# Kernel tuning notes

Measured on AMD Instinct MI355X. Metric: run time of the kernel, lower is better.

The kernel has to match this reference:

```python
import jax, jax.numpy as jnp
import numpy as np
from jax import lax

NUM_CHANNELS = 3
NUM_HEADS = 8
PATCH = 16  # projection_dim = 3 * 16 * 16 = 768
EPS = 1e-5


def setup_inputs() -> dict:
    key = jax.random.key(0)
    ks = jax.random.split(key, 16)
    B, N, D, Hdim = 4, 1024, 768, 3072
    H = NUM_HEADS

    def init(k, shape, fan_in):
        bound = 1.0 / np.sqrt(fan_in)
        return jax.random.uniform(k, shape, jnp.float32, -bound, bound)

    return {
        "x": jax.random.normal(ks[0], (B, N, D), jnp.float32),
        # 3x3 conv QKV projections over per-patch [3,16,16] images (no bias, qkv_bias=False)
        "qconv_w": init(ks[1], (NUM_CHANNELS, NUM_CHANNELS, 3, 3), NUM_CHANNELS * 9),
        "kconv_w": init(ks[2], (NUM_CHANNELS, NUM_CHANNELS, 3, 3), NUM_CHANNELS * 9),
        "vconv_w": init(ks[3], (NUM_CHANNELS, NUM_CHANNELS, 3, 3), NUM_CHANNELS * 9),
        # 1x1 conv mixing heads of the attention map + BatchNorm2d(heads)
        "reatten_w": init(ks[4], (H, H), H),
        "reatten_b": init(ks[5], (H,), H),
        "bn_g": jnp.ones((H,), jnp.float32),
        "bn_b": jnp.zeros((H,), jnp.float32),
        # output projection (Linear dim->dim)
        "proj_w": init(ks[6], (D, D), D),
        "proj_b": init(ks[7], (D,), D),
        # LayerNorm over (num_patches, projection_dim) jointly
        "ln_g": jnp.ones((N, D), jnp.float32),
        "ln_b": jnp.zeros((N, D), jnp.float32),
        # FeedForward
        "ff_w1": init(ks[8], (Hdim, D), D),
        "ff_b1": init(ks[9], (Hdim,), D),
        "ff_w2": init(ks[10], (D, Hdim), Hdim),
        "ff_b2": init(ks[11], (D,), Hdim),
    }


def _conv3x3(x, w):
    # x: [BN, C, p, p], w: [C, C, 3, 3], stride 1, SAME padding
    return lax.conv_general_dilated(x, w, (1, 1), "SAME",
                                    dimension_numbers=("NCHW", "OIHW", "NCHW"))


def _layernorm_2d(x, g, b):
    # LayerNorm over last two axes (N, D) jointly, biased variance, eps=1e-5
    mu = jnp.mean(x, axis=(-2, -1), keepdims=True)
    var = jnp.mean(jnp.square(x - mu), axis=(-2, -1), keepdims=True)
    return (x - mu) * lax.rsqrt(var + EPS) * g + b


def _encoder_fwd(x, qconv_w, kconv_w, vconv_w, reatten_w, reatten_b,
                 bn_g, bn_b, proj_w, proj_b, ln_g, ln_b,
                 ff_w1, ff_b1, ff_w2, ff_b2):
    B, N, D = x.shape
    H = NUM_HEADS
    hd = D // H
    scale = hd ** -0.5

    # --- ReAttention ---
    xi = x.reshape(B * N, NUM_CHANNELS, PATCH, PATCH)

    def qkv(w):
        y = _conv3x3(xi, w).reshape(B, N, H, hd)
        return y.transpose(0, 2, 1, 3)  # [B, H, N, hd]

    q, k, v = qkv(qconv_w), qkv(kconv_w), qkv(vconv_w)

    attn = jax.nn.softmax(jnp.einsum("bhnd,bhmd->bhnm", q, k) * scale, axis=-1)

    # learned cross-head 1x1 conv + BatchNorm2d (training-mode batch stats)
    attn = jnp.einsum("gh,bhnm->bgnm", reatten_w, attn) + reatten_b[None, :, None, None]
    mu = jnp.mean(attn, axis=(0, 2, 3), keepdims=True)
    var = jnp.mean(jnp.square(attn - mu), axis=(0, 2, 3), keepdims=True)
    attn = (attn - mu) * lax.rsqrt(var + EPS)
    attn = attn * bn_g[None, :, None, None] + bn_b[None, :, None, None]

    out = jnp.einsum("bhnm,bhmd->bhnd", attn, v)
    out = out.transpose(0, 2, 1, 3).reshape(B, N, D)
    out = out @ proj_w.T + proj_b

    # --- residual + LN ---
    x1 = _layernorm_2d(x + out, ln_g, ln_b)

    # --- FeedForward (exact GELU) + residual + LN ---
    h = jax.nn.gelu(x1 @ ff_w1.T + ff_b1, approximate=False)
    ff = h @ ff_w2.T + ff_b2
    return _layernorm_2d(x1 + ff, ln_g, ln_b)


def reference(x, qconv_w, kconv_w, vconv_w, reatten_w, reatten_b,
              bn_g, bn_b, proj_w, proj_b, ln_g, ln_b,
              ff_w1, ff_b1, ff_w2, ff_b2):
    return _encoder_fwd(x, qconv_w, kconv_w, vconv_w, reatten_w, reatten_b,
                        bn_g, bn_b, proj_w, proj_b, ln_g, ln_b,
                        ff_w1, ff_b1, ff_w2, ff_b2)
```

## Files before the change

kernel.cpp:

```cpp
#include <hip/hip_runtime.h>
#include <math.h>


typedef unsigned short u16;
typedef unsigned int u32;
typedef __bf16 bf16x8 __attribute__((ext_vector_type(8)));
typedef float f32x4 __attribute__((ext_vector_type(4)));

#define EPSV 1e-5f
#define SL2E 0.14724444620253177f
#define EXPC -11.541560327111707f

__device__ __forceinline__ u16 f2bf(float f) {
  union { float f; u32 u; } v; v.f = f;
  u32 u = v.u + 0x7fffu + ((v.u >> 16) & 1u);
  return (u16)(u >> 16);
}
__device__ __forceinline__ float bf2f(u16 h) {
  union { u32 u; float f; } v; v.u = ((u32)h) << 16; return v.f;
}
__device__ __forceinline__ f32x4 mfma16(bf16x8 a, bf16x8 b, f32x4 c) {
  return __builtin_amdgcn_mfma_f32_16x16x32_bf16(a, b, c, 0, 0, 0);
}
__device__ __forceinline__ void gload16(const void* gp, void* lp) {
  __builtin_amdgcn_global_load_lds(
      (const __attribute__((address_space(1))) u32*)gp,
      (__attribute__((address_space(3))) u32*)lp, 16, 0, 0);
}

__global__ __launch_bounds__(256) void k_f2b(const float* __restrict__ s,
                                             u16* __restrict__ d, int n) {
  int i = blockIdx.x * 256 + threadIdx.x;
  int stride = gridDim.x * 256;
  for (; i < n; i += stride) d[i] = f2bf(s[i]);
}

__global__ __launch_bounds__(256) void k_conv(const float* __restrict__ x,
    const float* __restrict__ wq, const float* __restrict__ wk, const float* __restrict__ wv,
    u16* __restrict__ qhi, u16* __restrict__ qlo,
    u16* __restrict__ khi, u16* __restrict__ klo,
    float* __restrict__ vb)
{
  __shared__ float patch[768], swq[81], swk[81], swv[81];
  int bid = blockIdx.x;
  int b = bid >> 10, n = bid & 1023;
  int t = threadIdx.x;
  const float* xr = x + (size_t)bid * 768;
  patch[t] = xr[t]; patch[t + 256] = xr[t + 256]; patch[t + 512] = xr[t + 512];
  if (t < 81) { swq[t] = wq[t]; swk[t] = wk[t]; swv[t] = wv[t]; }
  __syncthreads();
  #pragma unroll
  for (int r = 0; r < 3; ++r) {
    int f = t + 256 * r;
    int o = f >> 8, rem = f & 255, pp = rem >> 4, qq = rem & 15;
    float aq = 0.f, ak = 0.f, av = 0.f;
    #pragma unroll
    for (int i = 0; i < 3; ++i)
      #pragma unroll
      for (int dp = 0; dp < 3; ++dp) {
        int ip = pp + dp - 1;
        if (ip < 0 || ip > 15) continue;
        #pragma unroll
        for (int dq = 0; dq < 3; ++dq) {
          int iq = qq + dq - 1;
          if (iq < 0 || iq > 15) continue;
          float pv = patch[i * 256 + ip * 16 + iq];
          int wi = ((o * 3 + i) * 3 + dp) * 3 + dq;
          aq += swq[wi] * pv; ak += swk[wi] * pv; av += swv[wi] * pv;
        }
      }
    int h = f / 96, d = f - h * 96;
    size_t oi = ((size_t)(b * 8 + h) * 1024 + n) * 96 + d;
    float aqs = aq * SL2E;
    u16 qh_ = f2bf(aqs); qhi[oi] = qh_; qlo[oi] = f2bf(aqs - bf2f(qh_));
    u16 kh_ = f2bf(ak);  khi[oi] = kh_; klo[oi] = f2bf(ak - bf2f(kh_));
    vb[oi] = av;
  }
}

__global__ __launch_bounds__(256) void k_vtr(const float* __restrict__ vb,
                                             u16* __restrict__ vtr)
{
  __shared__ u16 lds[12288];
  int bid = blockIdx.x;
  int bh = bid >> 3, n0 = (bid & 7) * 128;
  int t = threadIdx.x;
  int n = t >> 1, dh = (t & 1) * 48;
  const float* src = vb + ((size_t)bh * 1024 + n0 + n) * 96 + dh;
  #pragma unroll
  for (int j4 = 0; j4 < 12; ++j4) {
    float4 v = *(const float4*)(src + j4 * 4);
    int d = dh + j4 * 4;
    lds[(d + 0) * 128 + n] = f2bf(v.x);
    lds[(d + 1) * 128 + n] = f2bf(v.y);
    lds[(d + 2) * 128 + n] = f2bf(v.z);
    lds[(d + 3) * 128 + n] = f2bf(v.w);
  }
  __syncthreads();
  #pragma unroll
  for (int j = 0; j < 48; ++j) {
    int flat = t + 256 * j;
    int d = flat >> 7, n2 = flat & 127;
    vtr[((size_t)bh * 96 + d) * 1024 + n0 + n2] = lds[flat];
  }
}

#define LOADK(KH, KL, M)                                            \
  {                                                                 \
    size_t ko_ = (kbase + (M) + l15) * 96 + (size_t)(lhi * 8);      \
    _Pragma("unroll")                                               \
    for (int kk = 0; kk < 3; ++kk) {                                \
      KH[kk] = *(const bf16x8*)(khi + ko_ + kk * 32);               \
      KL[kk] = *(const bf16x8*)(klo + ko_ + kk * 32);               \
    }                                                               \
  }

__global__ __launch_bounds__(256, 4) void k_passA(
    const u16* __restrict__ qhi, const u16* __restrict__ qlo,
    const u16* __restrict__ khi, const u16* __restrict__ klo,
    float* __restrict__ zp)
{
  int bid = blockIdx.x;
  int bh = bid >> 6, rest = bid & 63, tile = rest >> 2, qtr = rest & 3;
  int t = threadIdx.x, lane = t & 63, wv = t >> 6;
  int l15 = lane & 15, lhi = lane >> 4;
  int n0 = tile * 64 + wv * 16;
  size_t qoff = ((size_t)bh * 1024 + n0 + l15) * 96 + lhi * 8;
  bf16x8 qh[3], ql[3];
  #pragma unroll
  for (int kk = 0; kk < 3; ++kk) {
    qh[kk] = *(const bf16x8*)(qhi + qoff + kk * 32);
    ql[kk] = *(const bf16x8*)(qlo + qoff + kk * 32);
  }
  size_t kbase = (size_t)bh * 1024;
  float z[4] = {0.f, 0.f, 0.f, 0.f};
  bf16x8 khA[3], klA[3], khB[3], klB[3];
  int m0 = qtr * 256;
  LOADK(khA, klA, m0)
  for (int it = 0; it < 8; ++it) {
    int mb = m0 + it * 32;
    LOADK(khB, klB, mb + 16)
    {
      f32x4 C = {0.f, 0.f, 0.f, 0.f};
      #pragma unroll
      for (int kk = 0; kk < 3; ++kk) {
        C = mfma16(qh[kk], khA[kk], C);
        C = mfma16(qh[kk], klA[kk], C);
        C = mfma16(ql[kk], khA[kk], C);
      }
      #pragma unroll
      for (int r = 0; r < 4; ++r) z[r] += exp2f(C[r] + EXPC);
    }
    if (it < 7) LOADK(khA, klA, mb + 32)
    {
      f32x4 C = {0.f, 0.f, 0.f, 0.f};
      #pragma unroll
      for (int kk = 0; kk < 3; ++kk) {
        C = mfma16(qh[kk], khB[kk], C);
        C = mfma16(qh[kk], klB[kk], C);
        C = mfma16(ql[kk], khB[kk], C);
      }
      #pragma unroll
      for (int r = 0; r < 4; ++r) z[r] += exp2f(C[r] + EXPC);
    }
  }
  #pragma unroll
  for (int off = 1; off < 16; off <<= 1)
    #pragma unroll
    for (int r = 0; r < 4; ++r) z[r] += __shfl_xor(z[r], off);
  if (l15 == 0) {
    #pragma unroll
    for (int r = 0; r < 4; ++r)
      zp[qtr * 32768 + bh * 1024 + n0 + lhi * 4 + r] = z[r];
  }
}

__global__ __launch_bounds__(256) void k_zmerge(const float* __restrict__ zp,
                                                float* __restrict__ invZ)
{
  int idx = blockIdx.x * 256 + threadIdx.x;
  float z = zp[idx] + zp[32768 + idx] + zp[65536 + idx] + zp[98304 + idx];
  invZ[idx] = 1.f / z;
}

__global__ __launch_bounds__(512, 4) void k_passB(
    const u16* __restrict__ qhi, const u16* __restrict__ qlo,
    const u16* __restrict__ khi, const u16* __restrict__ klo,
    const u16* __restrict__ vtr, const float* __restrict__ invZ,
    const float* __restrict__ rw,
    float* __restrict__ U0, float* __restrict__ U1,
    float* __restrict__ U2, float* __restrict__ U3,
    float* __restrict__ pstat)
{
  __shared__ u16 clds[32768];
  int bid = blockIdx.x;
  int b = bid >> 8, rest = bid & 255, nt = rest >> 2, mq = rest & 3;
  int n0 = nt * 16;
  int t = threadIdx.x, lane = t & 63, w = t >> 6;
  int l15 = lane & 15, lhi = lane >> 4;
  int mbase = mq * 256 + w * 32;
  int mrow0 = mbase + ((l15 >> 2) * 8) + (l15 & 3);

  float cm[8][8];
  #pragma unroll
  for (int g = 0; g < 8; ++g) {
    float wsum = 0.f;
    #pragma unroll
    for (int h = 0; h < 8; ++h) wsum += rw[g * 8 + h];
    float cg = -wsum * (1.f / 1024.f);
    #pragma unroll
    for (int jj = 0; jj < 8; ++jj) cm[g][jj] = cg;
  }

  #pragma unroll 1
  for (int h = 0; h < 8; ++h) {
    size_t base = (size_t)(b * 8 + h) * 1024;
    const u16* qhp = qhi + (base + n0 + l15) * 96 + lhi * 8;
    const u16* qlp = qlo + (base + n0 + l15) * 96 + lhi * 8;
    const u16* khp = khi + (base + mrow0) * 96 + lhi * 8;
    const u16* klp = klo + (base + mrow0) * 96 + lhi * 8;
    f32x4 C0 = {0.f, 0.f, 0.f, 0.f}, C1 = {0.f, 0.f, 0.f, 0.f};
    #pragma unroll
    for (int kk = 0; kk < 3; ++kk) {
      bf16x8 qh8 = *(const bf16x8*)(qhp + kk * 32);
      bf16x8 ql8 = *(const bf16x8*)(qlp + kk * 32);
      bf16x8 kh0 = *(const bf16x8*)(khp + kk * 32);
      bf16x8 kl0 = *(const bf16x8*)(klp + kk * 32);
      bf16x8 kh1 = *(const bf16x8*)(khp + 384 + kk * 32);
      bf16x8 kl1 = *(const bf16x8*)(klp + 384 + kk * 32);
      C0 = mfma16(kh0, qh8, C0);
      C0 = mfma16(kl0, qh8, C0);
      C0 = mfma16(kh0, ql8, C0);
      C1 = mfma16(kh1, qh8, C1);
      C1 = mfma16(kl1, qh8, C1);
      C1 = mfma16(kh1, ql8, C1);
    }
    float iz = invZ[base + n0 + l15];
    #pragma unroll
    for (int r = 0; r < 4; ++r) {
      float p0 = exp2f(C0[r] + EXPC) * iz;
      float p1 = exp2f(C1[r] + EXPC) * iz;
      #pragma unroll
      for (int g = 0; g < 8; ++g) {
        float wgh = rw[g * 8 + h];
        cm[g][r]     += wgh * p0;
        cm[g][4 + r] += wgh * p1;
      }
    }
  }

  {
    float sc[8], scc[8];
    #pragma unroll
    for (int g = 0; g < 8; ++g) {
      float s = 0.f, ss = 0.f;
      #pragma unroll
      for (int jj = 0; jj < 8; ++jj) { float v = cm[g][jj]; s += v; ss += v * v; }
      sc[g] = s; scc[g] = ss;
    }
    #pragma unroll
    for (int off = 32; off > 0; off >>= 1)
      #pragma unroll
      for (int g = 0; g < 8; ++g) {
        sc[g] += __shfl_down(sc[g], off);
        scc[g] += __shfl_down(scc[g], off);
      }
    if (lane == 0) {
      #pragma unroll
      for (int g = 0; g < 8; ++g) {
        pstat[(size_t)(bid * 8 + w) * 16 + g] = sc[g];
        pstat[(size_t)(bid * 8 + w) * 16 + 8 + g] = scc[g];
      }
    }
  }

  #pragma unroll
  for (int g = 0; g < 8; ++g) {
    union { u16 us[8]; bf16x8 bv; } pk;
    #pragma unroll
    for (int jj = 0; jj < 8; ++jj) pk.us[jj] = f2bf(cm[g][jj]);
    *(bf16x8*)&clds[((w * 8 + g) * 64 + lane) * 8] = pk.bv;
  }
  __syncthreads();

  f32x4 acc[6];
  #pragma unroll
  for (int ds = 0; ds < 6; ++ds) acc[ds] = (f32x4){0.f, 0.f, 0.f, 0.f};
  size_t vbase = (size_t)(b * 8 + w) * 96;
  for (int mc = 0; mc < 8; ++mc) {
    bf16x8 af = *(const bf16x8*)&clds[((mc * 8 + w) * 64 + lane) * 8];
    int mof = mq * 256 + mc * 32 + lhi * 8;
    #pragma unroll
    for (int ds = 0; ds < 6; ++ds) {
      bf16x8 vf = *(const bf16x8*)(vtr + (vbase + ds * 16 + l15) * 1024 + mof);
      acc[ds] = mfma16(af, vf, acc[ds]);
    }
  }
  float* Uq = (mq == 0) ? U0 : (mq == 1) ? U1 : (mq == 2) ? U2 : U3;
  #pragma unroll
  for (int ds = 0; ds < 6; ++ds)
    #pragma unroll
    for (int r = 0; r < 4; ++r) {
      int n = lhi * 4 + r;
      Uq[((size_t)(b * 1024 + n0 + n)) * 768 + w * 96 + ds * 16 + l15] = acc[ds][r];
    }
}

__global__ __launch_bounds__(384) void k_vcs(const float* __restrict__ vb,
                                             float* __restrict__ vcs)
{
  __shared__ float part[4][96];
  int bh = blockIdx.x, t = threadIdx.x;
  int c = t % 96, g4 = t / 96;
  float a = 0.f;
  const float* vp = vb + (size_t)bh * 98304 + (size_t)g4 * 24576 + c;
  for (int m = 0; m < 256; ++m) a += vp[m * 96];
  part[g4][c] = a;
  __syncthreads();
  if (t < 96) vcs[bh * 96 + t] = part[0][t] + part[1][t] + part[2][t] + part[3][t];
}

__global__ __launch_bounds__(256) void k_statred1(const float* __restrict__ pstat,
                                                  float* __restrict__ pred)
{
  __shared__ float part[16][17];
  int bb = blockIdx.x, t = threadIdx.x;
  int j = t >> 4, s = t & 15;
  float a = 0.f;
  #pragma unroll
  for (int k2 = 0; k2 < 8; ++k2)
    a += pstat[(size_t)(bb * 128 + s + 16 * k2) * 16 + j];
  part[j][s] = a;
  __syncthreads();
  if (t < 16) {
    float v = 0.f;
    #pragma unroll
    for (int s2 = 0; s2 < 16; ++s2) v += part[t][s2];
    pred[bb * 16 + t] = v;
  }
}

__global__ __launch_bounds__(256) void k_statred2(const float* __restrict__ pred,
                                                  float* __restrict__ stats)
{
  __shared__ float part[16][17];
  int t = threadIdx.x;
  int j = t >> 4, s = t & 15;
  float a = 0.f;
  #pragma unroll
  for (int k2 = 0; k2 < 4; ++k2)
    a += pred[(size_t)(s + 16 * k2) * 16 + j];
  part[j][s] = a;
  __syncthreads();
  if (t < 16) {
    float v = 0.f;
    #pragma unroll
    for (int s2 = 0; s2 < 16; ++s2) v += part[t][s2];
    stats[t] = v;
  }
}

__global__ __launch_bounds__(256) void k_bnfin(const float* __restrict__ U0,
    const float* __restrict__ U1, const float* __restrict__ U2,
    const float* __restrict__ U3, const float* __restrict__ vcs,
    const float* __restrict__ stats, const float* __restrict__ bng,
    const float* __restrict__ bnb, u16* __restrict__ ubb)
{
  size_t idx = (size_t)blockIdx.x * 256 + threadIdx.x;
  int col = (int)(idx % 768); int i = (int)(idx / 768); int b = i >> 10;
  int g = col / 96, d = col - g * 96;
  const float cnt = 4194304.f;
  float mc = stats[g] / cnt;
  float var = stats[8 + g] / cnt - mc * mc;
  float sg = bng[g] * rsqrtf(var + EPSV);
  float tg = bnb[g] - sg * mc;
  float u = (U0[idx] + U1[idx]) + (U2[idx] + U3[idx]);
  ubb[idx] = f2bf(sg * u + tg * vcs[(b * 8 + g) * 96 + d]);
}

template<int GELU_, int RES_, int STATS_, int BF16OUT>
__global__ __launch_bounds__(256) void k_gemm(
    const u16* __restrict__ A, const u16* __restrict__ W,
    const float* __restrict__ bias, const float* __restrict__ res,
    float* __restrict__ out, u16* __restrict__ outb,
    int K, int Nc, float* __restrict__ stats)
{
  __shared__ u16 As[8192], Bs[8192];
  __shared__ float red[8];
  int t = threadIdx.x, lane = t & 63, wv = t >> 6;
  int l15 = lane & 15, lhi = lane >> 4;
  int i0 = blockIdx.y * 128, j0 = blockIdx.x * 128;
  int wr = wv >> 1, wc = wv & 1;
  f32x4 acc[4][4];
  #pragma unroll
  for (int mi = 0; mi < 4; ++mi)
    #pragma unroll
    for (int ni = 0; ni < 4; ++ni) acc[mi][ni] = (f32x4){0.f, 0.f, 0.f, 0.f};
  int rA = lane >> 3;
  int colel = 8 * ((lane & 7) ^ rA);
  for (int k0 = 0; k0 < K; k0 += 64) {
    if (k0) __syncthreads();
    #pragma unroll
    for (int i = 0; i < 4; ++i) {
      int cA = wv * 4 + i;
      int r = cA * 8 + rA;
      gload16(A + (size_t)(i0 + r) * K + k0 + colel, &As[cA * 512]);
      gload16(W + (size_t)(j0 + r) * K + k0 + colel, &Bs[cA * 512]);
    }
    __syncthreads();
    #pragma unroll
    for (int ks = 0; ks < 2; ++ks) {
      bf16x8 af[4], bf[4];
      #pragma unroll
      for (int mi = 0; mi < 4; ++mi) {
        int r2 = wr * 64 + mi * 16 + l15;
        af[mi] = *(const bf16x8*)&As[r2 * 64 + ((ks * 32 + lhi * 8) ^ (8 * (r2 & 7)))];
      }
      #pragma unroll
      for (int ni = 0; ni < 4; ++ni) {
        int r3 = wc * 64 + ni * 16 + l15;
        bf[ni] = *(const bf16x8*)&Bs[r3 * 64 + ((ks * 32 + lhi * 8) ^ (8 * (r3 & 7)))];
      }
      #pragma unroll
      for (int mi = 0; mi < 4; ++mi)
        #pragma unroll
        for (int ni = 0; ni < 4; ++ni)
          acc[mi][ni] = mfma16(af[mi], bf[ni], acc[mi][ni]);
    }
  }
  float ls = 0.f, lss = 0.f;
  #pragma unroll
  for (int mi = 0; mi < 4; ++mi) {
    #pragma unroll
    for (int ni = 0; ni < 4; ++ni) {
      int col = j0 + wc * 64 + ni * 16 + l15;
      float bv = bias[col];
      #pragma unroll
      for (int r = 0; r < 4; ++r) {
        int row = i0 + wr * 64 + mi * 16 + lhi * 4 + r;
        float val = acc[mi][ni][r] + bv;
        if (RES_) val += res[(size_t)row * Nc + col];
        if (GELU_) val = 0.5f * val * (1.f + erff(val * 0.70710678118654752f));
        if (BF16OUT) outb[(size_t)row * Nc + col] = f2bf(val);
        else out[(size_t)row * Nc + col] = val;
        if (STATS_) { ls += val; lss += val * val; }
      }
    }
  }
  if (STATS_) {
    #pragma unroll
    for (int off = 32; off > 0; off >>= 1) {
      ls += __shfl_down(ls, off); lss += __shfl_down(lss, off);
    }
    if (lane == 0) { red[wv * 2] = ls; red[wv * 2 + 1] = lss; }
    __syncthreads();
    if (t == 0) {
      int b = i0 >> 10;
      atomicAdd(&stats[b * 2],     red[0] + red[2] + red[4] + red[6]);
      atomicAdd(&stats[b * 2 + 1], red[1] + red[3] + red[5] + red[7]);
    }
  }
}

template<int BF16OUT>
__global__ __launch_bounds__(256) void k_ln(const float* __restrict__ y,
    const float* __restrict__ stats, const float* __restrict__ g,
    const float* __restrict__ bta, float* __restrict__ outp, u16* __restrict__ outb)
{
  size_t idx = (size_t)blockIdx.x * 256 + threadIdx.x;
  int i = (int)(idx / 768), col = (int)(idx % 768);
  int b = i >> 10, n = i & 1023;
  const float cnt = 786432.f;
  float mu = stats[b * 2] / cnt;
  float var = stats[b * 2 + 1] / cnt - mu * mu;
  float r = rsqrtf(var + EPSV);
  size_t gi = (size_t)n * 768 + col;
  float v = (y[idx] - mu) * r * g[gi] + bta[gi];
  outp[idx] = v;
  if (BF16OUT) outb[idx] = f2bf(v);
}

extern "C" void kernel_launch(void* const* d_in, const int* in_sizes, int n_in,
                              void* d_out, int out_size, void* d_ws, size_t ws_size,
                              hipStream_t stream)
{
  const float* x   = (const float*)d_in[0];
  const float* qw  = (const float*)d_in[1];
  const float* kw  = (const float*)d_in[2];
  const float* vw  = (const float*)d_in[3];
  const float* rw  = (const float*)d_in[4];
  const float* bng = (const float*)d_in[6];
  const float* bnb = (const float*)d_in[7];
  const float* pw  = (const float*)d_in[8];
  const float* pb  = (const float*)d_in[9];
  const float* lng = (const float*)d_in[10];
  const float* lnb = (const float*)d_in[11];
  const float* fw1 = (const float*)d_in[12];
  const float* fb1 = (const float*)d_in[13];
  const float* fw2 = (const float*)d_in[14];
  const float* fb2 = (const float*)d_in[15];
  float* out = (float*)d_out;

  float* ws    = (float*)d_ws;
  float* stats = ws;
  float* pstat = ws + 64;
  float* vcs   = ws + 131136;
  float* zp    = ws + 134208;
  float* invZ  = ws + 265280;
  float* vb    = ws + 298048;
  float* U0    = ws + 3443776;
  float* U1    = ws + 6589504;
  float* x1    = ws + 9735232;
  u16* u16b = (u16*)(ws + 12880960);
  u16* qhi  = u16b;
  u16* qlo  = u16b + 3145728;
  u16* khi  = u16b + 6291456;
  u16* klo  = u16b + 9437184;
  u16* vtr  = u16b + 12582912;
  u16* ubb  = u16b + 15728640;
  u16* pwb  = u16b + 18874368;
  u16* fw1b = u16b + 19464192;
  u16* fw2b = u16b + 21823488;
  float* U2 = vb;
  float* U3 = x1;
  float* pred = zp;
  u16* x1b = qhi;
  u16* hb  = qlo;
  float* y1 = U0;
  float* y2 = vb;

  hipMemsetAsync(stats, 0, 64 * sizeof(float), stream);
  k_f2b<<<1024, 256, 0, stream>>>(pw, pwb, 589824);
  k_f2b<<<2048, 256, 0, stream>>>(fw1, fw1b, 2359296);
  k_f2b<<<2048, 256, 0, stream>>>(fw2, fw2b, 2359296);

  k_conv<<<4096, 256, 0, stream>>>(x, qw, kw, vw, qhi, qlo, khi, klo, vb);
  k_passA<<<2048, 256, 0, stream>>>(qhi, qlo, khi, klo, zp);
  k_vtr<<<256, 256, 0, stream>>>(vb, vtr);
  k_vcs<<<32, 384, 0, stream>>>(vb, vcs);
  k_zmerge<<<128, 256, 0, stream>>>(zp, invZ);
  k_passB<<<1024, 512, 0, stream>>>(qhi, qlo, khi, klo, vtr, invZ, rw,
                                    U0, U1, U2, U3, pstat);
  k_statred1<<<64, 256, 0, stream>>>(pstat, pred);
  k_statred2<<<1, 256, 0, stream>>>(pred, stats);
  k_bnfin<<<12288, 256, 0, stream>>>(U0, U1, U2, U3, vcs, stats, bng, bnb, ubb);

  k_gemm<0,1,1,0><<<dim3(6, 32), 256, 0, stream>>>(ubb, pwb, pb, x, y1, nullptr, 768, 768, stats + 16);
  k_ln<1><<<12288, 256, 0, stream>>>(y1, stats + 16, lng, lnb, x1, x1b);
  k_gemm<1,0,0,1><<<dim3(24, 32), 256, 0, stream>>>(x1b, fw1b, fb1, nullptr, nullptr, hb, 768, 3072, nullptr);
  k_gemm<0,1,1,0><<<dim3(6, 32), 256, 0, stream>>>(hb, fw2b, fb2, x1, y2, nullptr, 3072, 768, stats + 24);
  k_ln<0><<<12288, 256, 0, stream>>>(y2, stats + 24, lng, lnb, out, nullptr);
}
```

Baseline: 373.4 us.

## Stage per-head probabilities in LDS and apply head mixing per output head

The passB kernel no longer keeps an 8x8 per-thread accumulator for all mixed heads across the head loop. Each wave now writes bf16 softmax probabilities for every head into LDS. Each wave then computes its own mixed head by combining the 8 heads per m-chunk just before the PV MFMA, which cuts register pressure and the 8x FMA fan-out per probability. The BatchNorm partial statistics become one value per wave per block, so the first stat-reduction kernel is simplified. The cost is that probabilities are rounded to bf16 before mixing rather than after, which adds a rounding step, and more LDS reads happen in the inner loop.

```diff
diff --git a/kernel.cpp b/kernel.cpp
--- a/kernel.cpp
+++ b/kernel.cpp
@@ -192,7 +192,7 @@
     float* __restrict__ U2, float* __restrict__ U3,
     float* __restrict__ pstat)
 {
-  __shared__ u16 clds[32768];
+  __shared__ u16 plds[32768];
   int bid = blockIdx.x;
   int b = bid >> 8, rest = bid & 255, nt = rest >> 2, mq = rest & 3;
   int n0 = nt * 16;
@@ -200,17 +200,6 @@
   int l15 = lane & 15, lhi = lane >> 4;
   int mbase = mq * 256 + w * 32;
   int mrow0 = mbase + ((l15 >> 2) * 8) + (l15 & 3);
-
-  float cm[8][8];
-  #pragma unroll
-  for (int g = 0; g < 8; ++g) {
-    float wsum = 0.f;
-    #pragma unroll
-    for (int h = 0; h < 8; ++h) wsum += rw[g * 8 + h];
-    float cg = -wsum * (1.f / 1024.f);
-    #pragma unroll
-    for (int jj = 0; jj < 8; ++jj) cm[g][jj] = cg;
-  }
 
   #pragma unroll 1
   for (int h = 0; h < 8; ++h) {
@@ -236,66 +225,64 @@
       C1 = mfma16(kh1, ql8, C1);
     }
     float iz = invZ[base + n0 + l15];
+    union { u16 us[8]; bf16x8 bv; } pk;
     #pragma unroll
     for (int r = 0; r < 4; ++r) {
-      float p0 = exp2f(C0[r] + EXPC) * iz;
-      float p1 = exp2f(C1[r] + EXPC) * iz;
-      #pragma unroll
-      for (int g = 0; g < 8; ++g) {
-        float wgh = rw[g * 8 + h];
-        cm[g][r]     += wgh * p0;
-        cm[g][4 + r] += wgh * p1;
-      }
-    }
-  }
-
-  {
-    float sc[8], scc[8];
-    #pragma unroll
-    for (int g = 0; g < 8; ++g) {
-      float s = 0.f, ss = 0.f;
-      #pragma unroll
-      for (int jj = 0; jj < 8; ++jj) { float v = cm[g][jj]; s += v; ss += v * v; }
-      sc[g] = s; scc[g] = ss;
-    }
-    #pragma unroll
-    for (int off = 32; off > 0; off >>= 1)
-      #pragma unroll
-      for (int g = 0; g < 8; ++g) {
-        sc[g] += __shfl_down(sc[g], off);
-        scc[g] += __shfl_down(scc[g], off);
-      }
-    if (lane == 0) {
-      #pragma unroll
-      for (int g = 0; g < 8; ++g) {
-        pstat[(size_t)(bid * 8 + w) * 16 + g] = sc[g];
-        pstat[(size_t)(bid * 8 + w) * 16 + 8 + g] = scc[g];
-      }
-    }
-  }
-
-  #pragma unroll
-  for (int g = 0; g < 8; ++g) {
+      pk.us[r]     = f2bf(exp2f(C0[r] + EXPC) * iz);
+      pk.us[4 + r] = f2bf(exp2f(C1[r] + EXPC) * iz);
+    }
+    *(bf16x8*)&plds[((w * 8 + h) * 64 + lane) * 8] = pk.bv;
+  }
+  __syncthreads();
+
+  float wg[8];
+  #pragma unroll
+  for (int h = 0; h < 8; ++h) wg[h] = rw[w * 8 + h];
+  float cg = -(((wg[0] + wg[1]) + (wg[2] + wg[3])) +
+               ((wg[4] + wg[5]) + (wg[6] + wg[7]))) * (1.f / 1024.f);
+  f32x4 acc[6];
+  #pragma unroll
+  for (int ds = 0; ds < 6; ++ds) acc[ds] = (f32x4){0.f, 0.f, 0.f, 0.f};
+  float sc = 0.f, scc = 0.f;
+  size_t vbase = (size_t)(b * 8 + w) * 96;
+  #pragma unroll 1
+  for (int mc = 0; mc < 8; ++mc) {
+    float cm8[8];
+    #pragma unroll
+    for (int jj = 0; jj < 8; ++jj) cm8[jj] = cg;
+    #pragma unroll
+    for (int h = 0; h < 8; ++h) {
+      union { u32 ud[4]; bf16x8 bv; } pf;
+      pf.bv = *(const bf16x8*)&plds[((mc * 8 + h) * 64 + lane) * 8];
+      float wgh = wg[h];
+      #pragma unroll
+      for (int k2 = 0; k2 < 4; ++k2) {
+        union { u32 u; float f; } lo, hi;
+        lo.u = pf.ud[k2] << 16;
+        hi.u = pf.ud[k2] & 0xffff0000u;
+        cm8[2 * k2]     += wgh * lo.f;
+        cm8[2 * k2 + 1] += wgh * hi.f;
+      }
+    }
     union { u16 us[8]; bf16x8 bv; } pk;
     #pragma unroll
-    for (int jj = 0; jj < 8; ++jj) pk.us[jj] = f2bf(cm[g][jj]);
-    *(bf16x8*)&clds[((w * 8 + g) * 64 + lane) * 8] = pk.bv;
-  }
-  __syncthreads();
-
-  f32x4 acc[6];
-  #pragma unroll
-  for (int ds = 0; ds < 6; ++ds) acc[ds] = (f32x4){0.f, 0.f, 0.f, 0.f};
-  size_t vbase = (size_t)(b * 8 + w) * 96;
-  for (int mc = 0; mc < 8; ++mc) {
-    bf16x8 af = *(const bf16x8*)&clds[((mc * 8 + w) * 64 + lane) * 8];
+    for (int jj = 0; jj < 8; ++jj) {
+      sc += cm8[jj]; scc += cm8[jj] * cm8[jj];
+      pk.us[jj] = f2bf(cm8[jj]);
+    }
     int mof = mq * 256 + mc * 32 + lhi * 8;
     #pragma unroll
     for (int ds = 0; ds < 6; ++ds) {
       bf16x8 vf = *(const bf16x8*)(vtr + (vbase + ds * 16 + l15) * 1024 + mof);
-      acc[ds] = mfma16(af, vf, acc[ds]);
-    }
-  }
+      acc[ds] = mfma16(pk.bv, vf, acc[ds]);
+    }
+  }
+  #pragma unroll
+  for (int off = 32; off > 0; off >>= 1) {
+    sc += __shfl_down(sc, off); scc += __shfl_down(scc, off);
+  }
+  if (lane == 0) { pstat[bid * 16 + w] = sc; pstat[bid * 16 + 8 + w] = scc; }
+
   float* Uq = (mq == 0) ? U0 : (mq == 1) ? U1 : (mq == 2) ? U2 : U3;
   #pragma unroll
   for (int ds = 0; ds < 6; ++ds)
@@ -326,11 +313,7 @@
   __shared__ float part[16][17];
   int bb = blockIdx.x, t = threadIdx.x;
   int j = t >> 4, s = t & 15;
-  float a = 0.f;
-  #pragma unroll
-  for (int k2 = 0; k2 < 8; ++k2)
-    a += pstat[(size_t)(bb * 128 + s + 16 * k2) * 16 + j];
-  part[j][s] = a;
+  part[j][s] = pstat[(size_t)(bb * 16 + s) * 16 + j];
   __syncthreads();
   if (t < 16) {
     float v = 0.f;
```

Measured after the change: 372.2 us. About the same (-0.3%).
